# Kernel optimization log

Hardware: AMD Instinct MI355X
Metric: run time of the kernel (lower is better)

## Reference

```python
import jax, jax.numpy as jnp
import numpy as np

B, L, D = 4, 2048, 1024
H, DK, DV = 16, 64, 64
EPS = 1e-6


def setup_inputs() -> dict:
    key = jax.random.key(0)
    ks = jax.random.split(key, 8)
    s = 0.02
    return {
        "q": jax.random.normal(ks[0], (B, L, D), dtype=jnp.float32),
        "k": jax.random.normal(ks[1], (B, L, D), dtype=jnp.float32),
        "v": jax.random.normal(ks[2], (B, L, D), dtype=jnp.float32),
        "Wq": jax.random.normal(ks[3], (H * DK, D), dtype=jnp.float32) * s,
        "Wk": jax.random.normal(ks[4], (H * DK, D), dtype=jnp.float32) * s,
        "Wv": jax.random.normal(ks[5], (H * DV, D), dtype=jnp.float32) * s,
        "Wfc": jax.random.normal(ks[6], (D, H * DV), dtype=jnp.float32) * s,
        "ln_g": jnp.ones((D,), dtype=jnp.float32),
        "ln_b": jnp.zeros((D,), dtype=jnp.float32),
    }


def reference(q, k, v, Wq, Wk, Wv, Wfc, ln_g, ln_b):
    residual = q
    # projections (Linear: x @ W.T), reshape to [B, H, L, d]
    qh = (q @ Wq.T).reshape(B, L, H, DK).transpose(0, 2, 1, 3)
    kh = (k @ Wk.T).reshape(B, L, H, DK).transpose(0, 2, 1, 3)
    vh = (v @ Wv.T).reshape(B, L, H, DV).transpose(0, 2, 1, 3)
    temperature = jnp.float32(DK) ** 0.5
    # scores [B, H, Lq, Lk]
    scores = jnp.einsum("bhqd,bhkd->bhqk", qh / temperature, kh)
    attn = jax.nn.softmax(scores, axis=-1)
    ctx = jnp.einsum("bhqk,bhkd->bhqd", attn, vh)  # [B, H, L, DV]
    ctx = ctx.transpose(0, 2, 1, 3).reshape(B, L, H * DV)
    out = ctx @ Wfc.T + residual
    # LayerNorm(eps=1e-6)
    mu = jnp.mean(out, axis=-1, keepdims=True)
    var = jnp.var(out, axis=-1, keepdims=True)
    out = (out - mu) * jax.lax.rsqrt(var + EPS) * ln_g + ln_b
    return out, attn
```

## Files before the change

kernel.cpp:

```cpp
#include <hip/hip_runtime.h>
#include <hip/hip_bf16.h>

typedef __bf16 bf16;
typedef __bf16 bf16x8 __attribute__((ext_vector_type(8)));
typedef __bf16 bf16x4 __attribute__((ext_vector_type(4)));
typedef __bf16 bf16x2 __attribute__((ext_vector_type(2)));
typedef float f32x4 __attribute__((ext_vector_type(4)));
typedef float f32x16 __attribute__((ext_vector_type(16)));
typedef unsigned int u32x4 __attribute__((ext_vector_type(4)));

#define MFMA_BF16(a, b, c) __builtin_amdgcn_mfma_f32_16x16x32_bf16((a), (b), (c), 0, 0, 0)
#define MFMA32(a, b, c) __builtin_amdgcn_mfma_f32_32x32x16_bf16((a), (b), (c), 0, 0, 0)

#if defined(__has_builtin)
#if __has_builtin(__builtin_amdgcn_exp2f)
#define EXP2F(x) __builtin_amdgcn_exp2f(x)
#endif
#endif
#ifndef EXP2F
#define EXP2F(x) exp2f(x)
#endif

static constexpr int Bc = 4, Lc = 2048, Dc = 1024, Hc = 16, DKc = 64;
static constexpr int BLc = Bc * Lc;
static constexpr float CEXP = 0.18033688011112042f;

__device__ inline unsigned pk2(float a, float b) {
  bf16x2 t;
  t[0] = (bf16)a;
  t[1] = (bf16)b;
  return __builtin_bit_cast(unsigned, t);
}

__global__ __launch_bounds__(256) void cvt_w(const float* __restrict__ src,
                                             bf16* __restrict__ dst) {
  int i = blockIdx.x * 256 + threadIdx.x;
  float4 f = ((const float4*)src)[i];
  bf16x4 o;
  o[0] = (bf16)f.x; o[1] = (bf16)f.y; o[2] = (bf16)f.z; o[3] = (bf16)f.w;
  *(bf16x4*)(dst + (size_t)i * 4) = o;
}

template <int A_F32, int OUT_MODE>
__global__ __launch_bounds__(256) void gemm128(const void* __restrict__ Av,
                                               const bf16* __restrict__ Bw,
                                               void* __restrict__ Cv,
                                               const float* __restrict__ resid) {
  __shared__ bf16 As[128][72];
  __shared__ bf16 Bs[128][72];
  const int t = threadIdx.x;
  const int lane = t & 63, wid = t >> 6;
  const int wr = wid >> 1, wc = wid & 1;
  const int m0 = blockIdx.x * 128, n0 = blockIdx.y * 128;
  const int sub = t & 7, srow = t >> 3;

  f32x4 acc[4][4] = {};

  for (int kt = 0; kt < 1024; kt += 64) {
    if (A_F32) {
      const float* A = (const float*)Av;
#pragma unroll
      for (int s = 0; s < 4; ++s) {
        int r = srow + 32 * s;
        const float4* pa = (const float4*)(A + (size_t)(m0 + r) * 1024 + kt + sub * 8);
        float4 f0 = pa[0], f1 = pa[1];
        bf16x8 o;
        o[0] = (bf16)f0.x; o[1] = (bf16)f0.y; o[2] = (bf16)f0.z; o[3] = (bf16)f0.w;
        o[4] = (bf16)f1.x; o[5] = (bf16)f1.y; o[6] = (bf16)f1.z; o[7] = (bf16)f1.w;
        *(bf16x8*)&As[r][sub * 8] = o;
      }
    } else {
      const bf16* A = (const bf16*)Av;
#pragma unroll
      for (int s = 0; s < 4; ++s) {
        int r = srow + 32 * s;
        u32x4 u = *(const u32x4*)(A + (size_t)(m0 + r) * 1024 + kt + sub * 8);
        *(u32x4*)&As[r][sub * 8] = u;
      }
    }
#pragma unroll
    for (int s = 0; s < 4; ++s) {
      int r = srow + 32 * s;
      u32x4 u = *(const u32x4*)(Bw + (size_t)(n0 + r) * 1024 + kt + sub * 8);
      *(u32x4*)&Bs[r][sub * 8] = u;
    }
    __syncthreads();
#pragma unroll
    for (int c = 0; c < 2; ++c) {
      const int ko = c * 32 + (lane >> 4) * 8;
      bf16x8 af[4], bfr[4];
#pragma unroll
      for (int m = 0; m < 4; ++m)
        af[m] = *(const bf16x8*)&As[wr * 64 + m * 16 + (lane & 15)][ko];
#pragma unroll
      for (int n = 0; n < 4; ++n)
        bfr[n] = *(const bf16x8*)&Bs[wc * 64 + n * 16 + (lane & 15)][ko];
#pragma unroll
      for (int m = 0; m < 4; ++m)
#pragma unroll
        for (int n = 0; n < 4; ++n)
          acc[m][n] = MFMA_BF16(af[m], bfr[n], acc[m][n]);
    }
    __syncthreads();
  }

  const int rbase = m0 + wr * 64 + (lane >> 4) * 4;
  const int cbase = n0 + wc * 64 + (lane & 15);
  if (OUT_MODE == 1) {
    float* C = (float*)Cv;
#pragma unroll
    for (int m = 0; m < 4; ++m)
#pragma unroll
      for (int n = 0; n < 4; ++n)
#pragma unroll
        for (int r = 0; r < 4; ++r) {
          size_t row = (size_t)(rbase + m * 16 + r);
          size_t col = (size_t)(cbase + n * 16);
          C[row * 1024 + col] = acc[m][n][r] + resid[row * 1024 + col];
        }
  } else if (OUT_MODE == 0) {
    bf16* C = (bf16*)Cv;
#pragma unroll
    for (int m = 0; m < 4; ++m)
#pragma unroll
      for (int n = 0; n < 4; ++n)
#pragma unroll
        for (int r = 0; r < 4; ++r) {
          size_t row = (size_t)(rbase + m * 16 + r);
          size_t col = (size_t)(cbase + n * 16);
          C[row * 1024 + col] = (bf16)acc[m][n][r];
        }
  } else {
    bf16* C = (bf16*)Cv;
#pragma unroll
    for (int m = 0; m < 4; ++m)
#pragma unroll
      for (int n = 0; n < 4; ++n)
#pragma unroll
        for (int r = 0; r < 4; ++r) {
          int row = rbase + m * 16 + r;
          int col = cbase + n * 16;
          size_t dst = ((size_t)((row >> 11) << 10) + col) * 2048 + (row & 2047);
          C[dst] = (bf16)acc[m][n][r];
        }
  }
}

__global__ __launch_bounds__(256, 3) void attn_kernel(const bf16* __restrict__ qh,
                                                      const bf16* __restrict__ kh,
                                                      const bf16* __restrict__ vt,
                                                      bf16* __restrict__ ctx,
                                                      float* __restrict__ attn_out) {
  __shared__ bf16 Ks[64][72];
  __shared__ bf16 Vs[64][72];
  const int t = threadIdx.x, lane = t & 63, w = t >> 6;
  const int hi = lane >> 5, ql = lane & 31;
  const int qt = blockIdx.x, h = blockIdx.y, b = blockIdx.z;
  const size_t rowbase = (size_t)b * 2048;
  const int qrow = qt * 128 + w * 32 + ql;
  const bf16* kbase = kh + rowbase * 1024 + h * 64;
  const bf16* vbase = vt + (size_t)(b * 16 + h) * 64 * 2048;
  const int sub = t & 7, srow = t >> 3;

  bf16x8 qf[4];
  {
    const bf16* qp = qh + (rowbase + qrow) * 1024 + h * 64 + hi * 8;
#pragma unroll
    for (int c = 0; c < 4; ++c) qf[c] = *(const bf16x8*)(qp + c * 16);
  }

  f32x16 cacc[2] = {};
  float zacc = 0.f;

  for (int kt = 0; kt < 2048; kt += 64) {
    __syncthreads();
#pragma unroll
    for (int s = 0; s < 2; ++s) {
      int r = srow + 32 * s;
      *(u32x4*)&Ks[r][sub * 8] =
          *(const u32x4*)(kbase + (size_t)(kt + r) * 1024 + sub * 8);
      *(u32x4*)&Vs[r][sub * 8] =
          *(const u32x4*)(vbase + (size_t)r * 2048 + kt + sub * 8);
    }
    __syncthreads();
#pragma unroll
    for (int sb = 0; sb < 2; ++sb) {
      f32x16 s = {};
#pragma unroll
      for (int c = 0; c < 4; ++c) {
        bf16x8 kf = *(const bf16x8*)&Ks[sb * 32 + ql][c * 16 + hi * 8];
        s = MFMA32(kf, qf[c], s);
      }
      float p[16];
#pragma unroll
      for (int j = 0; j < 16; ++j) {
        p[j] = EXP2F(s[j] * CEXP);
        zacc += p[j];
      }
      unsigned pv[4][2];
#pragma unroll
      for (int o = 0; o < 4; ++o)
#pragma unroll
        for (int d = 0; d < 2; ++d) pv[o][d] = pk2(p[o * 4 + 2 * d], p[o * 4 + 2 * d + 1]);
      bf16x8 pa[2];
#pragma unroll
      for (int c = 0; c < 2; ++c) {
        u32x4 pu;
#pragma unroll
        for (int d = 0; d < 2; ++d) {
          unsigned a = pv[2 * c][d], bq = pv[2 * c + 1][d];
          unsigned as = (unsigned)__shfl_xor((int)a, 32);
          unsigned bs = (unsigned)__shfl_xor((int)bq, 32);
          pu[d] = hi ? bs : a;
          pu[2 + d] = hi ? bq : as;
        }
        pa[c] = __builtin_bit_cast(bf16x8, pu);
      }
#pragma unroll
      for (int n = 0; n < 2; ++n)
#pragma unroll
        for (int c = 0; c < 2; ++c) {
          bf16x8 vf = *(const bf16x8*)&Vs[n * 32 + ql][sb * 32 + c * 16 + hi * 8];
          cacc[n] = MFMA32(pa[c], vf, cacc[n]);
        }
    }
  }

  float z = zacc + __shfl_xor(zacc, 32);
  float rz = 1.0f / z;

  {
    float rzv[16];
#pragma unroll
    for (int g = 0; g < 16; ++g)
      rzv[g] = __shfl(rz, (g & 3) + 8 * (g >> 2) + 4 * hi);
#pragma unroll
    for (int n = 0; n < 2; ++n)
#pragma unroll
      for (int g = 0; g < 16; ++g) {
        int crow = (g & 3) + 8 * (g >> 2) + 4 * hi;
        size_t row = rowbase + (size_t)(qt * 128 + w * 32 + crow);
        ctx[row * 1024 + h * 64 + n * 32 + ql] = (bf16)(cacc[n][g] * rzv[g]);
      }
  }

  float* abase = attn_out + ((size_t)(b * 16 + h) * 2048 + qrow) * 2048;
  for (int kt = 0; kt < 2048; kt += 64) {
#pragma unroll
    for (int sb = 0; sb < 2; ++sb) {
      f32x16 s = {};
      const bf16* kp = kbase + (size_t)(kt + sb * 32 + ql) * 1024 + hi * 8;
#pragma unroll
      for (int c = 0; c < 4; ++c) {
        bf16x8 kf = *(const bf16x8*)(kp + c * 16);
        s = MFMA32(kf, qf[c], s);
      }
#pragma unroll
      for (int o = 0; o < 4; ++o) {
        float4 v4;
        v4.x = EXP2F(s[o * 4 + 0] * CEXP) * rz;
        v4.y = EXP2F(s[o * 4 + 1] * CEXP) * rz;
        v4.z = EXP2F(s[o * 4 + 2] * CEXP) * rz;
        v4.w = EXP2F(s[o * 4 + 3] * CEXP) * rz;
        *(float4*)(abase + kt + sb * 32 + o * 8 + hi * 4) = v4;
      }
    }
  }
}

__global__ __launch_bounds__(256) void ln_kernel(float* __restrict__ io,
                                                 const float* __restrict__ g,
                                                 const float* __restrict__ bta) {
  const int row = blockIdx.x, t = threadIdx.x;
  float4* rp = (float4*)(io + (size_t)row * 1024);
  float4 v = rp[t];
  float s = v.x + v.y + v.z + v.w;
  float s2 = v.x * v.x + v.y * v.y + v.z * v.z + v.w * v.w;
#pragma unroll
  for (int off = 32; off >= 1; off >>= 1) {
    s += __shfl_xor(s, off);
    s2 += __shfl_xor(s2, off);
  }
  __shared__ float ls[4], ls2[4];
  const int w = t >> 6;
  if ((t & 63) == 0) { ls[w] = s; ls2[w] = s2; }
  __syncthreads();
  s = ls[0] + ls[1] + ls[2] + ls[3];
  s2 = ls2[0] + ls2[1] + ls2[2] + ls2[3];
  float mu = s * (1.f / 1024.f);
  float var = s2 * (1.f / 1024.f) - mu * mu;
  float rs = rsqrtf(var + 1e-6f);
  float4 gv = ((const float4*)g)[t];
  float4 bv = ((const float4*)bta)[t];
  v.x = (v.x - mu) * rs * gv.x + bv.x;
  v.y = (v.y - mu) * rs * gv.y + bv.y;
  v.z = (v.z - mu) * rs * gv.z + bv.z;
  v.w = (v.w - mu) * rs * gv.w + bv.w;
  rp[t] = v;
}

extern "C" void kernel_launch(void* const* d_in, const int* in_sizes, int n_in,
                              void* d_out, int out_size, void* d_ws, size_t ws_size,
                              hipStream_t stream) {
  (void)in_sizes; (void)n_in; (void)out_size; (void)ws_size;
  const float* q    = (const float*)d_in[0];
  const float* k    = (const float*)d_in[1];
  const float* v    = (const float*)d_in[2];
  const float* Wq   = (const float*)d_in[3];
  const float* Wk   = (const float*)d_in[4];
  const float* Wv   = (const float*)d_in[5];
  const float* Wfc  = (const float*)d_in[6];
  const float* ln_g = (const float*)d_in[7];
  const float* ln_b = (const float*)d_in[8];

  char* ws = (char*)d_ws;
  const size_t MB = 1024ull * 1024ull;
  bf16* wqb  = (bf16*)(ws + 0 * MB);
  bf16* wkb  = (bf16*)(ws + 2 * MB);
  bf16* wvb  = (bf16*)(ws + 4 * MB);
  bf16* wfcb = (bf16*)(ws + 6 * MB);
  bf16* qh   = (bf16*)(ws + 8 * MB);
  bf16* kh   = (bf16*)(ws + 24 * MB);
  bf16* vt   = (bf16*)(ws + 40 * MB);
  bf16* ctx  = (bf16*)(ws + 56 * MB);

  float* outp  = (float*)d_out;
  float* attnp = outp + (size_t)BLc * Dc;

  cvt_w<<<1024, 256, 0, stream>>>(Wq, wqb);
  cvt_w<<<1024, 256, 0, stream>>>(Wk, wkb);
  cvt_w<<<1024, 256, 0, stream>>>(Wv, wvb);
  cvt_w<<<1024, 256, 0, stream>>>(Wfc, wfcb);

  dim3 gg(64, 8);
  gemm128<1, 0><<<gg, 256, 0, stream>>>(q, wqb, qh, nullptr);
  gemm128<1, 0><<<gg, 256, 0, stream>>>(k, wkb, kh, nullptr);
  gemm128<1, 2><<<gg, 256, 0, stream>>>(v, wvb, vt, nullptr);

  attn_kernel<<<dim3(16, 16, 4), 256, 0, stream>>>(qh, kh, vt, ctx, attnp);

  gemm128<0, 1><<<gg, 256, 0, stream>>>(ctx, wfcb, outp, q);
  ln_kernel<<<8192, 256, 0, stream>>>(outp, ln_g, ln_b);
}
```

Measured before the change: 596.0 us.

## Use direct global-to-LDS loads with XOR swizzle in projection GEMMs

Converts q/k/v activations to bf16 in separate passes so every GEMM takes bf16 inputs. The GEMM is rewritten to stage tiles with global_load_lds (direct global-to-LDS) into an XOR-swizzled unpadded layout, and uses 8 waves of 512 threads with a 4x2 MFMA tile per wave. This is meant to cut register-staged copy overhead and LDS bank conflicts, at the cost of extra conversion kernels and additional memory traffic for the bf16 activation copies.

New measurement: 606.9 us. Within noise of the previous version (+1.8%).

```diff
diff --git a/kernel.cpp b/kernel.cpp
--- a/kernel.cpp
+++ b/kernel.cpp
@@ -32,86 +32,79 @@
   return __builtin_bit_cast(unsigned, t);
 }
 
-__global__ __launch_bounds__(256) void cvt_w(const float* __restrict__ src,
-                                             bf16* __restrict__ dst) {
-  int i = blockIdx.x * 256 + threadIdx.x;
-  float4 f = ((const float4*)src)[i];
-  bf16x4 o;
-  o[0] = (bf16)f.x; o[1] = (bf16)f.y; o[2] = (bf16)f.z; o[3] = (bf16)f.w;
-  *(bf16x4*)(dst + (size_t)i * 4) = o;
-}
-
-template <int A_F32, int OUT_MODE>
-__global__ __launch_bounds__(256) void gemm128(const void* __restrict__ Av,
+__device__ __forceinline__ void gload_lds16(const bf16* g, bf16* l) {
+  __builtin_amdgcn_global_load_lds(
+      (const __attribute__((address_space(1))) void*)g,
+      (__attribute__((address_space(3))) void*)l, 16, 0, 0);
+}
+
+__global__ __launch_bounds__(256) void cvt8(const float* __restrict__ src,
+                                            bf16* __restrict__ dst) {
+  size_t i = ((size_t)blockIdx.x * 256 + threadIdx.x) * 8;
+  float4 f0 = *(const float4*)(src + i);
+  float4 f1 = *(const float4*)(src + i + 4);
+  bf16x8 o;
+  o[0] = (bf16)f0.x; o[1] = (bf16)f0.y; o[2] = (bf16)f0.z; o[3] = (bf16)f0.w;
+  o[4] = (bf16)f1.x; o[5] = (bf16)f1.y; o[6] = (bf16)f1.z; o[7] = (bf16)f1.w;
+  *(bf16x8*)(dst + i) = o;
+}
+
+template <int OUT_MODE>
+__global__ __launch_bounds__(512) void gemm_gl(const bf16* __restrict__ A,
                                                const bf16* __restrict__ Bw,
                                                void* __restrict__ Cv,
                                                const float* __restrict__ resid) {
-  __shared__ bf16 As[128][72];
-  __shared__ bf16 Bs[128][72];
+  __shared__ bf16 As[128 * 64];
+  __shared__ bf16 Bs[128 * 64];
   const int t = threadIdx.x;
   const int lane = t & 63, wid = t >> 6;
-  const int wr = wid >> 1, wc = wid & 1;
+  const int wr = wid >> 2, wc = wid & 3;
   const int m0 = blockIdx.x * 128, n0 = blockIdx.y * 128;
-  const int sub = t & 7, srow = t >> 3;
-
-  f32x4 acc[4][4] = {};
+  const int srow = lane >> 3, sslot = lane & 7;
+
+  f32x4 acc[4][2] = {};
 
   for (int kt = 0; kt < 1024; kt += 64) {
-    if (A_F32) {
-      const float* A = (const float*)Av;
-#pragma unroll
-      for (int s = 0; s < 4; ++s) {
-        int r = srow + 32 * s;
-        const float4* pa = (const float4*)(A + (size_t)(m0 + r) * 1024 + kt + sub * 8);
-        float4 f0 = pa[0], f1 = pa[1];
-        bf16x8 o;
-        o[0] = (bf16)f0.x; o[1] = (bf16)f0.y; o[2] = (bf16)f0.z; o[3] = (bf16)f0.w;
-        o[4] = (bf16)f1.x; o[5] = (bf16)f1.y; o[6] = (bf16)f1.z; o[7] = (bf16)f1.w;
-        *(bf16x8*)&As[r][sub * 8] = o;
-      }
-    } else {
-      const bf16* A = (const bf16*)Av;
-#pragma unroll
-      for (int s = 0; s < 4; ++s) {
-        int r = srow + 32 * s;
-        u32x4 u = *(const u32x4*)(A + (size_t)(m0 + r) * 1024 + kt + sub * 8);
-        *(u32x4*)&As[r][sub * 8] = u;
-      }
-    }
-#pragma unroll
-    for (int s = 0; s < 4; ++s) {
-      int r = srow + 32 * s;
-      u32x4 u = *(const u32x4*)(Bw + (size_t)(n0 + r) * 1024 + kt + sub * 8);
-      *(u32x4*)&Bs[r][sub * 8] = u;
+#pragma unroll
+    for (int a = 0; a < 2; ++a) {
+      const int rbase = a * 64 + wid * 8;
+      const int row = rbase + srow;
+      const int scol = (sslot ^ (row & 7)) * 8;
+      gload_lds16(A + (size_t)(m0 + row) * 1024 + kt + scol, As + rbase * 64 + lane * 8);
+      gload_lds16(Bw + (size_t)(n0 + row) * 1024 + kt + scol, Bs + rbase * 64 + lane * 8);
     }
     __syncthreads();
 #pragma unroll
     for (int c = 0; c < 2; ++c) {
-      const int ko = c * 32 + (lane >> 4) * 8;
-      bf16x8 af[4], bfr[4];
+      const int cb = c * 64 + (lane >> 4) * 16;
+      bf16x8 af[4], bfr[2];
+#pragma unroll
+      for (int m = 0; m < 4; ++m) {
+        int row = wr * 64 + m * 16 + (lane & 15);
+        af[m] = *(const bf16x8*)((const char*)As + row * 128 + (cb ^ ((row & 7) << 4)));
+      }
+#pragma unroll
+      for (int n = 0; n < 2; ++n) {
+        int row = wc * 32 + n * 16 + (lane & 15);
+        bfr[n] = *(const bf16x8*)((const char*)Bs + row * 128 + (cb ^ ((row & 7) << 4)));
+      }
 #pragma unroll
       for (int m = 0; m < 4; ++m)
-        af[m] = *(const bf16x8*)&As[wr * 64 + m * 16 + (lane & 15)][ko];
-#pragma unroll
-      for (int n = 0; n < 4; ++n)
-        bfr[n] = *(const bf16x8*)&Bs[wc * 64 + n * 16 + (lane & 15)][ko];
-#pragma unroll
-      for (int m = 0; m < 4; ++m)
-#pragma unroll
-        for (int n = 0; n < 4; ++n)
+#pragma unroll
+        for (int n = 0; n < 2; ++n)
           acc[m][n] = MFMA_BF16(af[m], bfr[n], acc[m][n]);
     }
     __syncthreads();
   }
 
   const int rbase = m0 + wr * 64 + (lane >> 4) * 4;
-  const int cbase = n0 + wc * 64 + (lane & 15);
+  const int cbase = n0 + wc * 32 + (lane & 15);
   if (OUT_MODE == 1) {
     float* C = (float*)Cv;
 #pragma unroll
     for (int m = 0; m < 4; ++m)
 #pragma unroll
-      for (int n = 0; n < 4; ++n)
+      for (int n = 0; n < 2; ++n)
 #pragma unroll
         for (int r = 0; r < 4; ++r) {
           size_t row = (size_t)(rbase + m * 16 + r);
@@ -123,7 +116,7 @@
 #pragma unroll
     for (int m = 0; m < 4; ++m)
 #pragma unroll
-      for (int n = 0; n < 4; ++n)
+      for (int n = 0; n < 2; ++n)
 #pragma unroll
         for (int r = 0; r < 4; ++r) {
           size_t row = (size_t)(rbase + m * 16 + r);
@@ -135,7 +128,7 @@
 #pragma unroll
     for (int m = 0; m < 4; ++m)
 #pragma unroll
-      for (int n = 0; n < 4; ++n)
+      for (int n = 0; n < 2; ++n)
 #pragma unroll
         for (int r = 0; r < 4; ++r) {
           int row = rbase + m * 16 + r;
@@ -319,26 +312,32 @@
   bf16* wkb  = (bf16*)(ws + 2 * MB);
   bf16* wvb  = (bf16*)(ws + 4 * MB);
   bf16* wfcb = (bf16*)(ws + 6 * MB);
-  bf16* qh   = (bf16*)(ws + 8 * MB);
-  bf16* kh   = (bf16*)(ws + 24 * MB);
-  bf16* vt   = (bf16*)(ws + 40 * MB);
-  bf16* ctx  = (bf16*)(ws + 56 * MB);
+  bf16* qb   = (bf16*)(ws + 8 * MB);
+  bf16* kb   = (bf16*)(ws + 24 * MB);
+  bf16* vb   = (bf16*)(ws + 40 * MB);
+  bf16* qh   = (bf16*)(ws + 56 * MB);
+  bf16* kh   = (bf16*)(ws + 72 * MB);
+  bf16* vt   = (bf16*)(ws + 88 * MB);
+  bf16* ctx  = (bf16*)(ws + 104 * MB);
 
   float* outp  = (float*)d_out;
   float* attnp = outp + (size_t)BLc * Dc;
 
-  cvt_w<<<1024, 256, 0, stream>>>(Wq, wqb);
-  cvt_w<<<1024, 256, 0, stream>>>(Wk, wkb);
-  cvt_w<<<1024, 256, 0, stream>>>(Wv, wvb);
-  cvt_w<<<1024, 256, 0, stream>>>(Wfc, wfcb);
+  cvt8<<<512, 256, 0, stream>>>(Wq, wqb);
+  cvt8<<<512, 256, 0, stream>>>(Wk, wkb);
+  cvt8<<<512, 256, 0, stream>>>(Wv, wvb);
+  cvt8<<<512, 256, 0, stream>>>(Wfc, wfcb);
+  cvt8<<<4096, 256, 0, stream>>>(q, qb);
+  cvt8<<<4096, 256, 0, stream>>>(k, kb);
+  cvt8<<<4096, 256, 0, stream>>>(v, vb);
 
   dim3 gg(64, 8);
-  gemm128<1, 0><<<gg, 256, 0, stream>>>(q, wqb, qh, nullptr);
-  gemm128<1, 0><<<gg, 256, 0, stream>>>(k, wkb, kh, nullptr);
-  gemm128<1, 2><<<gg, 256, 0, stream>>>(v, wvb, vt, nullptr);
+  gemm_gl<0><<<gg, 512, 0, stream>>>(qb, wqb, qh, nullptr);
+  gemm_gl<0><<<gg, 512, 0, stream>>>(kb, wkb, kh, nullptr);
+  gemm_gl<2><<<gg, 512, 0, stream>>>(vb, wvb, vt, nullptr);
 
   attn_kernel<<<dim3(16, 16, 4), 256, 0, stream>>>(qh, kh, vt, ctx, attnp);
 
-  gemm128<0, 1><<<gg, 256, 0, stream>>>(ctx, wfcb, outp, q);
+  gemm_gl<1><<<gg, 512, 0, stream>>>(ctx, wfcb, outp, q);
   ln_kernel<<<8192, 256, 0, stream>>>(outp, ln_g, ln_b);
 }
```
